# Optimization experiments

Measured on AMD Instinct MI355X. Metric: run time of the kernel, lower is better.

The kernel has to match this reference:

```python
import jax, jax.numpy as jnp
import numpy as np

M_POOL = 12500  # rows of the down_transform sparse matrix


def setup_inputs() -> dict:
    key = jax.random.key(0)
    ks = jax.random.split(key, 6)
    B, N, E, Cin, Cout, K, P = 4, 50000, 800000, 32, 64, 6, 50000
    x = jax.random.normal(ks[0], (B, N, Cin), jnp.float32)
    edge_index = jax.random.randint(ks[1], (2, E), 0, N, dtype=jnp.int64)
    pool_row = jax.random.randint(ks[2], (P,), 0, M_POOL, dtype=jnp.int64)
    pool_col = jax.random.randint(ks[3], (P,), 0, N, dtype=jnp.int64)
    pool_val = jax.random.uniform(ks[4], (P,), jnp.float32)
    # xavier_uniform over each [Cin, Cout] slice; bias zero-init (reset_parameters)
    limit = np.sqrt(6.0 / (Cin + Cout)).astype(np.float32)
    weight = jax.random.uniform(ks[5], (K, Cin, Cout), jnp.float32, -limit, limit)
    bias = jnp.zeros((Cout,), jnp.float32)
    return dict(x=x, edge_index=edge_index, pool_row=pool_row,
                pool_col=pool_col, pool_val=pool_val, weight=weight, bias=bias)


def _cheb_conv(x, edge_index, weight, bias):
    # x: [B, N, Cin]; weight: [K, Cin, Cout]
    N = x.shape[1]
    row, col = edge_index[0], edge_index[1]
    ones = jnp.ones(row.shape, x.dtype)
    deg = jax.ops.segment_sum(ones, row, num_segments=N)
    dis = jnp.where(deg > 0, jax.lax.rsqrt(jnp.where(deg > 0, deg, 1.0)), 0.0)
    # L_hat = 2L/lambda_max - I with lambda_max=2, sym norm -> diag 0, off-diag -d_i^-1/2 d_j^-1/2
    norm = -dis[row] * dis[col]  # [E]

    def prop(h):  # h: [B, N, C] -> L_hat @ h (gather, scale, scatter_add)
        msgs = h[:, col, :] * norm[None, :, None]  # [B, E, C]
        return jnp.zeros_like(h).at[:, row, :].add(msgs)

    Tx0 = x
    out = jnp.einsum('bnc,co->bno', Tx0, weight[0])
    Tx1 = prop(Tx0)
    out = out + jnp.einsum('bnc,co->bno', Tx1, weight[1])
    for k in range(2, weight.shape[0]):
        Tx2 = 2.0 * prop(Tx1) - Tx0
        out = out + jnp.einsum('bnc,co->bno', Tx2, weight[k])
        Tx0, Tx1 = Tx1, Tx2
    return out + bias


def reference(x, edge_index, pool_row, pool_col, pool_val, weight, bias):
    h = _cheb_conv(x, edge_index, weight, bias)  # single block (n_blocks=1)
    h = jax.nn.elu(h)
    # Pool: gather columns, scale by sparse values, scatter_add into rows
    B, _, C = h.shape
    gathered = h[:, pool_col, :] * pool_val[None, :, None]  # [B, P, C]
    out = jnp.zeros((B, M_POOL, C), h.dtype).at[:, pool_row, :].add(gathered)
    return out
```

## Files before the change

kernel.cpp:

```cpp
#include <hip/hip_runtime.h>
#include <hip/hip_fp16.h>
#include <cstdint>

#define N_NODES 50000
#define B_SZ 4
#define C_IN 32
#define C_OUT 64
#define K_CHEB 6
#define M_POOL 12500
#define NT_ROWS (N_NODES + M_POOL)
#define NS32 ((size_t)N_NODES * C_IN)
#define ZH ((size_t)N_NODES * C_OUT)
#define CN_CAP 2048
#define DSTR 16
#define NWELEM (K_CHEB * 4 * 64 * 8)

typedef _Float16 f16x8 __attribute__((ext_vector_type(8)));
typedef float f32x4 __attribute__((ext_vector_type(4)));
typedef unsigned int u32x4 __attribute__((ext_vector_type(4)));
typedef unsigned short ushort_t;

__device__ __forceinline__ unsigned short f2h(float f) {
    union { _Float16 h; unsigned short u; } v;
    v.h = (_Float16)f;
    return v.u;
}

__device__ __forceinline__ float h2f(unsigned short u) {
    union { unsigned short u; _Float16 h; } v;
    v.u = u;
    return (float)v.h;
}

__device__ __forceinline__ __half2 u2h2(unsigned u) { return __builtin_bit_cast(__half2, u); }
__device__ __forceinline__ unsigned h22u(__half2 h) { return __builtin_bit_cast(unsigned, h); }

__global__ void zero_deg_kernel(int* __restrict__ deg_s) {
    int i = blockIdx.x * 256 + threadIdx.x;
    if (i < NT_ROWS * DSTR) deg_s[i] = 0;
}

__global__ void deg_slot_kernel(const int* __restrict__ row, const int* __restrict__ prow,
                                int* __restrict__ deg_s, int* __restrict__ slot, int E, int P) {
    int e = blockIdx.x * blockDim.x + threadIdx.x;
    if (e < E) slot[e] = atomicAdd(&deg_s[row[e] * DSTR], 1);
    else if (e < E + P) slot[e] = atomicAdd(&deg_s[(N_NODES + prow[e - E]) * DSTR], 1);
}

__global__ void disdegp_bsum_kernel(const int* __restrict__ deg_s, float* __restrict__ dis,
                                    int* __restrict__ degp, int* __restrict__ bsum) {
    __shared__ int sm[256];
    int i = blockIdx.x * 256 + threadIdx.x;
    int dp = 0;
    if (i < N_NODES) {
        int d = deg_s[i * DSTR];
        dis[i] = d > 0 ? rsqrtf((float)d) : 0.f;
        dp = (d + 7) & ~7;
        degp[i] = dp;
    } else if (i < NT_ROWS) {
        dp = deg_s[i * DSTR];
        degp[i] = dp;
    }
    sm[threadIdx.x] = dp;
    __syncthreads();
    for (int s = 128; s > 0; s >>= 1) {
        if (threadIdx.x < s) sm[threadIdx.x] += sm[threadIdx.x + s];
        __syncthreads();
    }
    if (threadIdx.x == 0) bsum[blockIdx.x] = sm[0];
}

__global__ void scan_bsum_kernel(int* bsum, int nb, int* rowptr, int N) {
    __shared__ int sm[256];
    int t = threadIdx.x;
    int v = (t < nb) ? bsum[t] : 0;
    sm[t] = v;
    __syncthreads();
    for (int off = 1; off < 256; off <<= 1) {
        int u = (t >= off) ? sm[t - off] : 0;
        __syncthreads();
        sm[t] += u;
        __syncthreads();
    }
    if (t < nb) bsum[t] = sm[t] - v;
    if (t == 0) rowptr[N] = sm[255];
}

__global__ void rowptr_kernel(const int* __restrict__ degp, const int* __restrict__ bsum,
                              int* __restrict__ rowptr, int N) {
    __shared__ int sm[256];
    int i = blockIdx.x * 256 + threadIdx.x;
    int t = threadIdx.x;
    int v = (i < N) ? degp[i] : 0;
    sm[t] = v;
    __syncthreads();
    for (int off = 1; off < 256; off <<= 1) {
        int u = (t >= off) ? sm[t - off] : 0;
        __syncthreads();
        sm[t] += u;
        __syncthreads();
    }
    if (i < N) rowptr[i] = bsum[blockIdx.x] + sm[t] - v;
}

__global__ void place_pad_kernel(const int* __restrict__ row, const int* __restrict__ col,
                                 const int* __restrict__ prow, const int* __restrict__ pcol,
                                 const float* __restrict__ pval, const float* __restrict__ dis,
                                 const int* __restrict__ rowptr, const int* __restrict__ slot,
                                 const int* __restrict__ deg_s,
                                 int2* __restrict__ cn, int E, int P) {
    int e = blockIdx.x * blockDim.x + threadIdx.x;
    if (e < E) {
        int r = row[e], c = col[e];
        float nm = -dis[r] * dis[c];
        unsigned h = f2h(nm);
        cn[rowptr[r] + slot[e]] = make_int2(c, (int)(h | (h << 16)));
    } else if (e < E + P) {
        int i = e - E;
        int r = N_NODES + prow[i];
        cn[rowptr[r] + slot[e]] = make_int2(pcol[i], __float_as_int(pval[i]));
    } else if (e < E + P + N_NODES) {
        int r = e - E - P;
        int p = rowptr[r] + deg_s[r * DSTR];
        int p1 = rowptr[r + 1];
        for (; p < p1; ++p) cn[p] = make_int2(0, 0);
    }
}

__global__ void packW_cast_kernel(const float* __restrict__ W, ushort_t* __restrict__ Wp,
                                  const float* __restrict__ xin, unsigned int* __restrict__ xout,
                                  int n2) {
    int i = blockIdx.x * 256 + threadIdx.x;
    if (i < NWELEM) {
        int j = i & 7;
        int lane = (i >> 3) & 63;
        int t = (i >> 9) & 3;
        int s = i >> 11;
        int k = (lane >> 4) * 8 + j;
        int colw = t * 16 + (lane & 15);
        Wp[i] = f2h(W[((size_t)s * C_IN + k) * C_OUT + colw]);
    } else {
        int c = i - NWELEM;
        if (c < n2) {
            unsigned a = f2h(xin[2 * c]), b = f2h(xin[2 * c + 1]);
            xout[c] = a | (b << 16);
        }
    }
}

__global__ void __launch_bounds__(256, 8)
prop_kernel(const ushort_t* __restrict__ hf, const ushort_t* __restrict__ p2f,
            ushort_t* __restrict__ outf,
            const int* __restrict__ rowptr, const int2* __restrict__ cn, float alpha) {
    __shared__ int2 lcn[CN_CAP];
    int bid = blockIdx.x;
    int b = bid & 3;
    int grp = bid >> 2;
    int r0 = grp * 64;
    int rend = r0 + 64 > N_NODES ? N_NODES : r0 + 64;
    int pbase = rowptr[r0];
    int pend = rowptr[rend];
    int cnt = pend - pbase;
    bool use_lds = (cnt <= CN_CAP);
    if (use_lds) {
        for (int i = threadIdx.x; i < cnt; i += 256) {
            unsigned long long u =
                __builtin_nontemporal_load((const unsigned long long*)(cn + pbase + i));
            lcn[i] = make_int2((int)(unsigned)(u & 0xffffffffULL), (int)(unsigned)(u >> 32));
        }
    }
    __syncthreads();

    int lr = threadIdx.x >> 2;
    int cs = threadIdx.x & 3;
    int r = r0 + lr;
    if (r >= N_NODES) return;
    const char* hb = (const char*)hf + (size_t)b * NS32 * 2;
    unsigned coff = (unsigned)cs * 16u;
    __half2 a0 = __float2half2_rn(0.f), a1 = a0, a2 = a0, a3 = a0;

    if (use_lds) {
        int p0 = rowptr[r] - pbase, p1 = rowptr[r + 1] - pbase;
        for (int p = p0; p < p1; p += 8) {
            unsigned off[8];
            __half2 n[8];
#pragma unroll
            for (int i = 0; i < 8; i++) {
                int2 e = lcn[p + i];
                off[i] = ((unsigned)e.x << 6) + coff;
                n[i] = u2h2((unsigned)e.y);
            }
            uint4 v[8];
#pragma unroll
            for (int i = 0; i < 8; i++) v[i] = *(const uint4*)(hb + off[i]);
#pragma unroll
            for (int i = 0; i < 8; i++) {
                a0 = __hfma2(u2h2(v[i].x), n[i], a0);
                a1 = __hfma2(u2h2(v[i].y), n[i], a1);
                a2 = __hfma2(u2h2(v[i].z), n[i], a2);
                a3 = __hfma2(u2h2(v[i].w), n[i], a3);
            }
        }
    } else {
        int p0 = rowptr[r], p1 = rowptr[r + 1];
        for (int p = p0; p < p1; p += 8) {
            unsigned off[8];
            __half2 n[8];
#pragma unroll
            for (int i = 0; i < 8; i++) {
                int2 e = cn[p + i];
                off[i] = ((unsigned)e.x << 6) + coff;
                n[i] = u2h2((unsigned)e.y);
            }
            uint4 v[8];
#pragma unroll
            for (int i = 0; i < 8; i++) v[i] = *(const uint4*)(hb + off[i]);
#pragma unroll
            for (int i = 0; i < 8; i++) {
                a0 = __hfma2(u2h2(v[i].x), n[i], a0);
                a1 = __hfma2(u2h2(v[i].y), n[i], a1);
                a2 = __hfma2(u2h2(v[i].z), n[i], a2);
                a3 = __hfma2(u2h2(v[i].w), n[i], a3);
            }
        }
    }

    unsigned ooff = ((unsigned)r << 6) + coff;
    u32x4 o;
    if (p2f) {
        __half2 al2 = __float2half2_rn(alpha);
        u32x4 pv = __builtin_nontemporal_load(
            (const u32x4*)((const char*)p2f + (size_t)b * NS32 * 2 + ooff));
        o[0] = h22u(__hfma2(a0, al2, __hneg2(u2h2(pv[0]))));
        o[1] = h22u(__hfma2(a1, al2, __hneg2(u2h2(pv[1]))));
        o[2] = h22u(__hfma2(a2, al2, __hneg2(u2h2(pv[2]))));
        o[3] = h22u(__hfma2(a3, al2, __hneg2(u2h2(pv[3]))));
    } else {
        o[0] = h22u(a0); o[1] = h22u(a1); o[2] = h22u(a2); o[3] = h22u(a3);
    }
    __builtin_nontemporal_store(o, (u32x4*)((char*)outf + (size_t)b * NS32 * 2 + ooff));
}

__global__ void gemm_mfma_kernel(const ushort_t* __restrict__ T0, const ushort_t* __restrict__ T1,
                                 const ushort_t* __restrict__ T2, const ushort_t* __restrict__ T3,
                                 const ushort_t* __restrict__ T4, const ushort_t* __restrict__ T5,
                                 const ushort_t* __restrict__ Wp,
                                 const float* __restrict__ bias, ushort_t* __restrict__ z) {
    int lane = threadIdx.x & 63;
    int wave = (blockIdx.x << 2) + (threadIdx.x >> 6);
    int r0 = wave << 4;
    int ga = r0 + (lane & 15);
    int koff = (lane >> 4) * 8;
    const ushort_t* Ts[6] = {T0, T1, T2, T3, T4, T5};

    f16x8 afr[6];
#pragma unroll
    for (int s = 0; s < 6; s++)
        afr[s] = *(const f16x8*)(Ts[s] + (size_t)ga * C_IN + koff);

    int orow = r0 + ((lane >> 4) << 2);
#pragma unroll
    for (int t = 0; t < 4; t++) {
        f32x4 acc = {0.f, 0.f, 0.f, 0.f};
#pragma unroll
        for (int s = 0; s < 6; s++) {
            f16x8 bfr = *(const f16x8*)(Wp + ((s * 4 + t) * 64 + lane) * 8);
            acc = __builtin_amdgcn_mfma_f32_16x16x32_f16(afr[s], bfr, acc, 0, 0, 0);
        }
        int col = (t << 4) + (lane & 15);
        float bv = bias[col];
#pragma unroll
        for (int rg = 0; rg < 4; rg++) {
            float v = acc[rg] + bv;
            z[(size_t)(orow + rg) * C_OUT + col] = f2h(v > 0.f ? v : (expf(v) - 1.f));
        }
    }
}

__global__ void pool_csr_kernel(const ushort_t* __restrict__ z, const int* __restrict__ rowptr,
                                const int2* __restrict__ cn, float* __restrict__ out) {
    int bid = blockIdx.x;
    int b = bid & 3;
    int r = (bid >> 2) * 8 + (threadIdx.x >> 5);
    int c2 = threadIdx.x & 31;
    if (r >= M_POOL) return;
    const char* zb = (const char*)z + (size_t)b * ZH * 2;
    unsigned coff = (unsigned)c2 << 2;
    float s0 = 0.f, s1 = 0.f;
    int p0 = rowptr[N_NODES + r], p1 = rowptr[N_NODES + r + 1];
    for (int p = p0; p < p1; ++p) {
        unsigned long long eu =
            __builtin_nontemporal_load((const unsigned long long*)(cn + p));
        unsigned ex = (unsigned)(eu & 0xffffffffULL);
        float v = __uint_as_float((unsigned)(eu >> 32));
        unsigned u = *(const unsigned*)(zb + ((ex << 7) + coff));
        s0 += h2f((ushort_t)u) * v;
        s1 += h2f((ushort_t)(u >> 16)) * v;
    }
    size_t idx = (size_t)b * M_POOL * C_OUT + (size_t)r * C_OUT + 2 * c2;
    *(float2*)&out[idx] = make_float2(s0, s1);
}

extern "C" void kernel_launch(void* const* d_in, const int* in_sizes, int n_in,
                              void* d_out, int out_size, void* d_ws, size_t ws_size,
                              hipStream_t stream) {
    const float* x    = (const float*)d_in[0];
    const int*   ei   = (const int*)d_in[1];
    const int*   prow = (const int*)d_in[2];
    const int*   pcol = (const int*)d_in[3];
    const float* pval = (const float*)d_in[4];
    const float* W    = (const float*)d_in[5];
    const float* bias = (const float*)d_in[6];
    const int E = in_sizes[1] / 2;
    const int P = in_sizes[2];
    const int* row = ei;
    const int* col = ei + E;
    const int EP_MAX = E + 7 * N_NODES + P;

    char* ws = (char*)d_ws;
    size_t o = 0;
    auto alloc = [&](size_t bytes) -> char* {
        char* p = ws + o;
        o += (bytes + 255) & ~(size_t)255;
        return p;
    };
    int nb = (NT_ROWS + 255) / 256;
    int*   deg_s  = (int*)alloc((size_t)NT_ROWS * DSTR * 4);
    int*   degp   = (int*)alloc((size_t)NT_ROWS * 4);
    float* dis    = (float*)alloc((size_t)N_NODES * 4);
    int*   rowptr = (int*)alloc((size_t)(NT_ROWS + 1) * 4);
    int*   slot   = (int*)alloc((size_t)(E + P) * 4);
    int*   bsum   = (int*)alloc((size_t)nb * 4);
    int2*  cn     = (int2*)alloc((size_t)EP_MAX * 8);
    ushort_t* Wp  = (ushort_t*)alloc((size_t)NWELEM * 2);
    ushort_t* xh  = (ushort_t*)alloc((size_t)B_SZ * NS32 * 2);
    ushort_t* hA  = (ushort_t*)alloc((size_t)B_SZ * NS32 * 2);
    ushort_t* hB  = (ushort_t*)alloc((size_t)B_SZ * NS32 * 2);
    ushort_t* hC  = (ushort_t*)alloc((size_t)B_SZ * NS32 * 2);
    ushort_t* hD  = (ushort_t*)alloc((size_t)B_SZ * NS32 * 2);
    ushort_t* hE  = (ushort_t*)alloc((size_t)B_SZ * NS32 * 2);
    ushort_t* z   = (ushort_t*)alloc((size_t)B_SZ * ZH * 2);

    zero_deg_kernel<<<(NT_ROWS * DSTR + 255) / 256, 256, 0, stream>>>(deg_s);
    deg_slot_kernel<<<(E + P + 255) / 256, 256, 0, stream>>>(row, prow, deg_s, slot, E, P);
    disdegp_bsum_kernel<<<nb, 256, 0, stream>>>(deg_s, dis, degp, bsum);
    scan_bsum_kernel<<<1, 256, 0, stream>>>(bsum, nb, rowptr, NT_ROWS);
    rowptr_kernel<<<nb, 256, 0, stream>>>(degp, bsum, rowptr, NT_ROWS);
    place_pad_kernel<<<(E + P + N_NODES + 255) / 256, 256, 0, stream>>>(
        row, col, prow, pcol, pval, dis, rowptr, slot, deg_s, cn, E, P);
    int n2 = (int)(B_SZ * NS32 / 2);
    packW_cast_kernel<<<(NWELEM + n2 + 255) / 256, 256, 0, stream>>>(W, Wp, x,
                                                                     (unsigned int*)xh, n2);

    int prop_blocks = ((N_NODES + 63) / 64) * B_SZ;
    int gemm_blocks = (B_SZ * N_NODES) / 64;

    prop_kernel<<<prop_blocks, 256, 0, stream>>>(xh, nullptr, hA, rowptr, cn, 1.0f);
    prop_kernel<<<prop_blocks, 256, 0, stream>>>(hA, xh, hB, rowptr, cn, 2.0f);
    prop_kernel<<<prop_blocks, 256, 0, stream>>>(hB, hA, hC, rowptr, cn, 2.0f);
    prop_kernel<<<prop_blocks, 256, 0, stream>>>(hC, hB, hD, rowptr, cn, 2.0f);
    prop_kernel<<<prop_blocks, 256, 0, stream>>>(hD, hC, hE, rowptr, cn, 2.0f);
    gemm_mfma_kernel<<<gemm_blocks, 256, 0, stream>>>(xh, hA, hB, hC, hD, hE, Wp, bias, z);
    pool_csr_kernel<<<((M_POOL + 7) / 8) * B_SZ, 256, 0, stream>>>(z, rowptr, cn,
                                                                   (float*)d_out);
}
```

Measured before the change: 269.0 us.

## Fuse W-pack and x-cast into degree kernel, drop padded degree array and nontemporal hints

Merges the weight packing and the fp32→fp16 input cast into the degree/slot atomic kernel, which removes one launch and lets that independent work overlap with the atomics. The per-node degree counters are no longer padded to 16-int strides, so they sit densely in memory, which may raise atomic contention on shared cache lines while shrinking the zeroing work. Nontemporal loads and stores in the propagation and pool kernels are replaced by ordinary accesses, which changes cache behaviour for the edge list and feature buffers.

Measured after the change: 244.4 us. -9.2%, faster.

```diff
diff --git a/kernel.cpp b/kernel.cpp
--- a/kernel.cpp
+++ b/kernel.cpp
@@ -12,12 +12,10 @@
 #define NS32 ((size_t)N_NODES * C_IN)
 #define ZH ((size_t)N_NODES * C_OUT)
 #define CN_CAP 2048
-#define DSTR 16
 #define NWELEM (K_CHEB * 4 * 64 * 8)
 
 typedef _Float16 f16x8 __attribute__((ext_vector_type(8)));
 typedef float f32x4 __attribute__((ext_vector_type(4)));
-typedef unsigned int u32x4 __attribute__((ext_vector_type(4)));
 typedef unsigned short ushort_t;
 
 __device__ __forceinline__ unsigned short f2h(float f) {
@@ -35,30 +33,54 @@
 __device__ __forceinline__ __half2 u2h2(unsigned u) { return __builtin_bit_cast(__half2, u); }
 __device__ __forceinline__ unsigned h22u(__half2 h) { return __builtin_bit_cast(unsigned, h); }
 
-__global__ void zero_deg_kernel(int* __restrict__ deg_s) {
+__global__ void zero_deg_kernel(int* __restrict__ deg) {
     int i = blockIdx.x * 256 + threadIdx.x;
-    if (i < NT_ROWS * DSTR) deg_s[i] = 0;
-}
-
-__global__ void deg_slot_kernel(const int* __restrict__ row, const int* __restrict__ prow,
-                                int* __restrict__ deg_s, int* __restrict__ slot, int E, int P) {
+    if (i < NT_ROWS) deg[i] = 0;
+}
+
+__global__ void build_pack_cast_kernel(const int* __restrict__ row, const int* __restrict__ prow,
+                                       int* __restrict__ deg, int* __restrict__ slot,
+                                       const float* __restrict__ W, ushort_t* __restrict__ Wp,
+                                       const float* __restrict__ xin,
+                                       unsigned int* __restrict__ xout,
+                                       int E, int P, int n2) {
     int e = blockIdx.x * blockDim.x + threadIdx.x;
-    if (e < E) slot[e] = atomicAdd(&deg_s[row[e] * DSTR], 1);
-    else if (e < E + P) slot[e] = atomicAdd(&deg_s[(N_NODES + prow[e - E]) * DSTR], 1);
-}
-
-__global__ void disdegp_bsum_kernel(const int* __restrict__ deg_s, float* __restrict__ dis,
+    if (e < E) {
+        slot[e] = atomicAdd(&deg[row[e]], 1);
+    } else if (e < E + P) {
+        slot[e] = atomicAdd(&deg[N_NODES + prow[e - E]], 1);
+    } else {
+        int i = e - (E + P);
+        if (i < NWELEM) {
+            int j = i & 7;
+            int lane = (i >> 3) & 63;
+            int t = (i >> 9) & 3;
+            int s = i >> 11;
+            int k = (lane >> 4) * 8 + j;
+            int colw = t * 16 + (lane & 15);
+            Wp[i] = f2h(W[((size_t)s * C_IN + k) * C_OUT + colw]);
+        } else {
+            int c = i - NWELEM;
+            if (c < n2) {
+                unsigned a = f2h(xin[2 * c]), b = f2h(xin[2 * c + 1]);
+                xout[c] = a | (b << 16);
+            }
+        }
+    }
+}
+
+__global__ void disdegp_bsum_kernel(const int* __restrict__ deg, float* __restrict__ dis,
                                     int* __restrict__ degp, int* __restrict__ bsum) {
     __shared__ int sm[256];
     int i = blockIdx.x * 256 + threadIdx.x;
     int dp = 0;
     if (i < N_NODES) {
-        int d = deg_s[i * DSTR];
+        int d = deg[i];
         dis[i] = d > 0 ? rsqrtf((float)d) : 0.f;
         dp = (d + 7) & ~7;
         degp[i] = dp;
     } else if (i < NT_ROWS) {
-        dp = deg_s[i * DSTR];
+        dp = deg[i];
         degp[i] = dp;
     }
     sm[threadIdx.x] = dp;
@@ -107,7 +129,7 @@
                                  const int* __restrict__ prow, const int* __restrict__ pcol,
                                  const float* __restrict__ pval, const float* __restrict__ dis,
                                  const int* __restrict__ rowptr, const int* __restrict__ slot,
-                                 const int* __restrict__ deg_s,
+                                 const int* __restrict__ deg,
                                  int2* __restrict__ cn, int E, int P) {
     int e = blockIdx.x * blockDim.x + threadIdx.x;
     if (e < E) {
@@ -121,30 +143,9 @@
         cn[rowptr[r] + slot[e]] = make_int2(pcol[i], __float_as_int(pval[i]));
     } else if (e < E + P + N_NODES) {
         int r = e - E - P;
-        int p = rowptr[r] + deg_s[r * DSTR];
+        int p = rowptr[r] + deg[r];
         int p1 = rowptr[r + 1];
         for (; p < p1; ++p) cn[p] = make_int2(0, 0);
-    }
-}
-
-__global__ void packW_cast_kernel(const float* __restrict__ W, ushort_t* __restrict__ Wp,
-                                  const float* __restrict__ xin, unsigned int* __restrict__ xout,
-                                  int n2) {
-    int i = blockIdx.x * 256 + threadIdx.x;
-    if (i < NWELEM) {
-        int j = i & 7;
-        int lane = (i >> 3) & 63;
-        int t = (i >> 9) & 3;
-        int s = i >> 11;
-        int k = (lane >> 4) * 8 + j;
-        int colw = t * 16 + (lane & 15);
-        Wp[i] = f2h(W[((size_t)s * C_IN + k) * C_OUT + colw]);
-    } else {
-        int c = i - NWELEM;
-        if (c < n2) {
-            unsigned a = f2h(xin[2 * c]), b = f2h(xin[2 * c + 1]);
-            xout[c] = a | (b << 16);
-        }
     }
 }
 
@@ -163,11 +164,7 @@
     int cnt = pend - pbase;
     bool use_lds = (cnt <= CN_CAP);
     if (use_lds) {
-        for (int i = threadIdx.x; i < cnt; i += 256) {
-            unsigned long long u =
-                __builtin_nontemporal_load((const unsigned long long*)(cn + pbase + i));
-            lcn[i] = make_int2((int)(unsigned)(u & 0xffffffffULL), (int)(unsigned)(u >> 32));
-        }
+        for (int i = threadIdx.x; i < cnt; i += 256) lcn[i] = cn[pbase + i];
     }
     __syncthreads();
 
@@ -226,19 +223,18 @@
     }
 
     unsigned ooff = ((unsigned)r << 6) + coff;
-    u32x4 o;
+    uint4 o;
     if (p2f) {
         __half2 al2 = __float2half2_rn(alpha);
-        u32x4 pv = __builtin_nontemporal_load(
-            (const u32x4*)((const char*)p2f + (size_t)b * NS32 * 2 + ooff));
-        o[0] = h22u(__hfma2(a0, al2, __hneg2(u2h2(pv[0]))));
-        o[1] = h22u(__hfma2(a1, al2, __hneg2(u2h2(pv[1]))));
-        o[2] = h22u(__hfma2(a2, al2, __hneg2(u2h2(pv[2]))));
-        o[3] = h22u(__hfma2(a3, al2, __hneg2(u2h2(pv[3]))));
+        uint4 pv = *(const uint4*)((const char*)p2f + (size_t)b * NS32 * 2 + ooff);
+        o.x = h22u(__hfma2(a0, al2, __hneg2(u2h2(pv.x))));
+        o.y = h22u(__hfma2(a1, al2, __hneg2(u2h2(pv.y))));
+        o.z = h22u(__hfma2(a2, al2, __hneg2(u2h2(pv.z))));
+        o.w = h22u(__hfma2(a3, al2, __hneg2(u2h2(pv.w))));
     } else {
-        o[0] = h22u(a0); o[1] = h22u(a1); o[2] = h22u(a2); o[3] = h22u(a3);
-    }
-    __builtin_nontemporal_store(o, (u32x4*)((char*)outf + (size_t)b * NS32 * 2 + ooff));
+        o.x = h22u(a0); o.y = h22u(a1); o.z = h22u(a2); o.w = h22u(a3);
+    }
+    *(uint4*)((char*)outf + (size_t)b * NS32 * 2 + ooff) = o;
 }
 
 __global__ void gemm_mfma_kernel(const ushort_t* __restrict__ T0, const ushort_t* __restrict__ T1,
@@ -289,11 +285,9 @@
     float s0 = 0.f, s1 = 0.f;
     int p0 = rowptr[N_NODES + r], p1 = rowptr[N_NODES + r + 1];
     for (int p = p0; p < p1; ++p) {
-        unsigned long long eu =
-            __builtin_nontemporal_load((const unsigned long long*)(cn + p));
-        unsigned ex = (unsigned)(eu & 0xffffffffULL);
-        float v = __uint_as_float((unsigned)(eu >> 32));
-        unsigned u = *(const unsigned*)(zb + ((ex << 7) + coff));
+        int2 e = cn[p];
+        float v = __int_as_float(e.y);
+        unsigned u = *(const unsigned*)(zb + (((unsigned)e.x << 7) + coff));
         s0 += h2f((ushort_t)u) * v;
         s1 += h2f((ushort_t)(u >> 16)) * v;
     }
@@ -325,7 +319,7 @@
         return p;
     };
     int nb = (NT_ROWS + 255) / 256;
-    int*   deg_s  = (int*)alloc((size_t)NT_ROWS * DSTR * 4);
+    int*   deg    = (int*)alloc((size_t)NT_ROWS * 4);
     int*   degp   = (int*)alloc((size_t)NT_ROWS * 4);
     float* dis    = (float*)alloc((size_t)N_NODES * 4);
     int*   rowptr = (int*)alloc((size_t)(NT_ROWS + 1) * 4);
@@ -341,16 +335,16 @@
     ushort_t* hE  = (ushort_t*)alloc((size_t)B_SZ * NS32 * 2);
     ushort_t* z   = (ushort_t*)alloc((size_t)B_SZ * ZH * 2);
 
-    zero_deg_kernel<<<(NT_ROWS * DSTR + 255) / 256, 256, 0, stream>>>(deg_s);
-    deg_slot_kernel<<<(E + P + 255) / 256, 256, 0, stream>>>(row, prow, deg_s, slot, E, P);
-    disdegp_bsum_kernel<<<nb, 256, 0, stream>>>(deg_s, dis, degp, bsum);
+    int n2 = (int)(B_SZ * NS32 / 2);
+
+    zero_deg_kernel<<<nb, 256, 0, stream>>>(deg);
+    build_pack_cast_kernel<<<(E + P + NWELEM + n2 + 255) / 256, 256, 0, stream>>>(
+        row, prow, deg, slot, W, Wp, x, (unsigned int*)xh, E, P, n2);
+    disdegp_bsum_kernel<<<nb, 256, 0, stream>>>(deg, dis, degp, bsum);
     scan_bsum_kernel<<<1, 256, 0, stream>>>(bsum, nb, rowptr, NT_ROWS);
     rowptr_kernel<<<nb, 256, 0, stream>>>(degp, bsum, rowptr, NT_ROWS);
     place_pad_kernel<<<(E + P + N_NODES + 255) / 256, 256, 0, stream>>>(
-        row, col, prow, pcol, pval, dis, rowptr, slot, deg_s, cn, E, P);
-    int n2 = (int)(B_SZ * NS32 / 2);
-    packW_cast_kernel<<<(NWELEM + n2 + 255) / 256, 256, 0, stream>>>(W, Wp, x,
-                                                                     (unsigned int*)xh, n2);
+        row, col, prow, pcol, pval, dis, rowptr, slot, deg, cn, E, P);
 
     int prop_blocks = ((N_NODES + 63) / 64) * B_SZ;
     int gemm_blocks = (B_SZ * N_NODES) / 64;
```
